# Optimization experiments

Hardware: AMD Instinct MI355X
Metric: run time of the kernel (lower is better)

Reference implementation:

```python
import jax, jax.numpy as jnp
import numpy as np

NEG = jnp.float32(-1e30)  # max-plus identity (finite to keep grads clean)


def setup_inputs() -> dict:
    key = jax.random.key(0)
    k1, k2 = jax.random.split(key)
    B, Cin, H, W = 8, 64, 64, 64
    Cout, kH, kW = 64, 3, 3
    x = jax.random.normal(k1, (B, Cin, H, W), dtype=jnp.float32)
    weight = jax.random.normal(k2, (Cout, Cin, kH, kW), dtype=jnp.float32)
    return {"x": x, "weight": weight, "kernel_size": 3, "padding": 1}


def reference(x, weight, kernel_size, padding):
    # Max-plus correlation (tropical conv), stride 1:
    #   out[b,co,y,x] = max_{ci,i,j} ( x_pad[b,ci,y+i,x+j] + weight[co,ci,i,j] )
    kH = kW = int(kernel_size)
    padH = padW = int(padding)
    B, Cin, H, W = x.shape
    Cout = weight.shape[0]
    xp = jnp.pad(x, ((0, 0), (0, 0), (padH, padH), (padW, padW)),
                 constant_values=NEG)  # -inf-like padding: identity of max
    Ho = H + 2 * padH - kH + 1
    Wo = W + 2 * padW - kW + 1
    out = jnp.full((B, Cout, Ho, Wo), NEG, dtype=x.dtype)
    for i in range(kH):          # small fixed kernel loop (kH*kW taps)
        for j in range(kW):
            win = xp[:, :, i:i + Ho, j:j + Wo]            # [B,Ci,Ho,Wo]
            cand = win[:, None] + weight[None, :, :, i, j, None, None]
            out = jnp.maximum(out, cand.max(axis=2))      # reduce over Ci
    return out
```

## Files before the change

kernel.cpp:

```cpp
#include <hip/hip_runtime.h>

#define NEGV -1e30f

constexpr int Bn = 8, Ci = 64, Hn = 64, Wn = 64, Co = 64;

constexpr int COB = 8;
constexpr int HT  = 4;

__global__ __launch_bounds__(256, 4)
void maxconv_kernel(const float* __restrict__ x, const float* __restrict__ wt,
                    float* __restrict__ out) {
    const int lane = threadIdx.x & 63;
    const int wrow = threadIdx.x >> 6;
    const int co0  = blockIdx.x * COB;
    const int h    = blockIdx.y * HT + wrow;
    const int b    = blockIdx.z;

    const int cl = lane > 0      ? lane - 1 : 0;
    const int cr = lane < Wn - 1 ? lane + 1 : Wn - 1;
    const bool edgeL = (lane == 0);
    const bool edgeR = (lane == Wn - 1);
    const bool hasUp = (h > 0);
    const bool hasDn = (h < Hn - 1);

    float acc[COB];
#pragma unroll
    for (int c = 0; c < COB; c++) acc[c] = NEGV;

    const float* p = x + ((size_t)b * Ci * Hn + h) * Wn;

    for (int ci = 0; ci < Ci; ci++, p += Hn * Wn) {
        float lm1 = NEGV, xm1 = NEGV, rm1 = NEGV;
        float lp1 = NEGV, xp1 = NEGV, rp1 = NEGV;
        if (hasUp) { lm1 = p[cl - Wn]; xm1 = p[lane - Wn]; rm1 = p[cr - Wn]; }
        if (hasDn) { lp1 = p[cl + Wn]; xp1 = p[lane + Wn]; rp1 = p[cr + Wn]; }
        float l0 = p[cl], x0 = p[lane], r0 = p[cr];

        if (edgeL) { lm1 = NEGV; l0 = NEGV; lp1 = NEGV; }
        if (edgeR) { rm1 = NEGV; r0 = NEGV; rp1 = NEGV; }

#pragma unroll
        for (int c = 0; c < COB; c++) {
            const float* wp = wt + ((size_t)(co0 + c) * Ci + ci) * 9;
            float t0 = lm1 + wp[0];
            float t1 = xm1 + wp[1];
            float t2 = rm1 + wp[2];
            float t3 = l0  + wp[3];
            float t4 = x0  + wp[4];
            float t5 = r0  + wp[5];
            float t6 = lp1 + wp[6];
            float t7 = xp1 + wp[7];
            float t8 = rp1 + wp[8];
            float a = acc[c];
            a = fmaxf(a, fmaxf(t0, t1));
            a = fmaxf(a, fmaxf(t2, t3));
            a = fmaxf(a, fmaxf(t4, t5));
            a = fmaxf(a, fmaxf(t6, t7));
            a = fmaxf(a, t8);
            acc[c] = a;
        }
    }

#pragma unroll
    for (int c = 0; c < COB; c++) {
        out[(((size_t)b * Co + co0 + c) * Hn + h) * Wn + lane] = acc[c];
    }
}

extern "C" void kernel_launch(void* const* d_in, const int* in_sizes, int n_in,
                              void* d_out, int out_size, void* d_ws, size_t ws_size,
                              hipStream_t stream) {
    const float* x  = (const float*)d_in[0];
    const float* wt = (const float*)d_in[1];
    float* out = (float*)d_out;

    dim3 grid(Co / COB, Hn / HT, Bn);
    maxconv_kernel<<<grid, 256, 0, stream>>>(x, wt, out);
}
```

Baseline: 125.4 us.

## Remap lanes to output channels with wave-uniform input loads and transposed weights

Restructures the work split so each wavefront lane handles one output channel while the wave covers a 4-wide strip of output columns. The input window values are then wave-uniform and can be scalar-loaded. A separate pre-pass transposes the weights so that per-lane weight loads are coalesced across output channels. Results are written as float4 stores. The aim is to drop the redundant per-channel weight loads and the divergent edge handling of the old layout, at the cost of an extra small kernel launch, workspace use, and output stores strided across channels.

```diff
diff --git a/kernel.cpp b/kernel.cpp
--- a/kernel.cpp
+++ b/kernel.cpp
@@ -4,67 +4,102 @@
 
 constexpr int Bn = 8, Ci = 64, Hn = 64, Wn = 64, Co = 64;
 
-constexpr int COB = 8;
-constexpr int HT  = 4;
+constexpr int G  = 4;
+constexpr int CW = Wn / G;
 
-__global__ __launch_bounds__(256, 4)
-void maxconv_kernel(const float* __restrict__ x, const float* __restrict__ wt,
-                    float* __restrict__ out) {
-    const int lane = threadIdx.x & 63;
-    const int wrow = threadIdx.x >> 6;
-    const int co0  = blockIdx.x * COB;
-    const int h    = blockIdx.y * HT + wrow;
-    const int b    = blockIdx.z;
+__global__ __launch_bounds__(256)
+void wtrans_kernel(const float* __restrict__ wt, float* __restrict__ wT) {
+    int idx = blockIdx.x * 256 + threadIdx.x;
+    if (idx < Ci * 9 * Co) {
+        int co = idx & 63;
+        int k  = (idx >> 6) % 9;
+        int ci = idx / (9 * Co);
+        wT[idx] = wt[((size_t)co * Ci + ci) * 9 + k];
+    }
+}
 
-    const int cl = lane > 0      ? lane - 1 : 0;
-    const int cr = lane < Wn - 1 ? lane + 1 : Wn - 1;
-    const bool edgeL = (lane == 0);
-    const bool edgeR = (lane == Wn - 1);
+template<int EDGE>
+__device__ __forceinline__ void load6(float* xv, const float* __restrict__ p) {
+    if (EDGE == 1) {
+        xv[0] = NEGV;
+#pragma unroll
+        for (int c = 1; c < 6; c++) xv[c] = p[c - 1];
+    } else if (EDGE == 2) {
+#pragma unroll
+        for (int c = 0; c < 5; c++) xv[c] = p[c];
+        xv[5] = NEGV;
+    } else {
+#pragma unroll
+        for (int c = 0; c < 6; c++) xv[c] = p[c];
+    }
+}
+
+template<int EDGE>
+__device__ __forceinline__ void run_wave(const float* __restrict__ x,
+                                         const float* __restrict__ wT,
+                                         float* __restrict__ out,
+                                         int b, int h, int w0, int lane) {
     const bool hasUp = (h > 0);
     const bool hasDn = (h < Hn - 1);
+    const int  cb    = (EDGE == 1) ? 0 : (w0 - 1);
 
-    float acc[COB];
+    const float* px = x + (((size_t)b * Ci) * Hn + h) * Wn + cb;
+    const float* pw = wT + lane;
+
+    float a[G];
 #pragma unroll
-    for (int c = 0; c < COB; c++) acc[c] = NEGV;
+    for (int p = 0; p < G; p++) a[p] = NEGV;
 
-    const float* p = x + ((size_t)b * Ci * Hn + h) * Wn;
+    for (int ci = 0; ci < Ci; ci++, px += Hn * Wn, pw += 9 * Co) {
+        float xu[6], xc[6], xd[6];
+        load6<EDGE>(xc, px);
+        if (hasUp) load6<EDGE>(xu, px - Wn);
+        else {
+#pragma unroll
+            for (int c = 0; c < 6; c++) xu[c] = NEGV;
+        }
+        if (hasDn) load6<EDGE>(xd, px + Wn);
+        else {
+#pragma unroll
+            for (int c = 0; c < 6; c++) xd[c] = NEGV;
+        }
 
-    for (int ci = 0; ci < Ci; ci++, p += Hn * Wn) {
-        float lm1 = NEGV, xm1 = NEGV, rm1 = NEGV;
-        float lp1 = NEGV, xp1 = NEGV, rp1 = NEGV;
-        if (hasUp) { lm1 = p[cl - Wn]; xm1 = p[lane - Wn]; rm1 = p[cr - Wn]; }
-        if (hasDn) { lp1 = p[cl + Wn]; xp1 = p[lane + Wn]; rp1 = p[cr + Wn]; }
-        float l0 = p[cl], x0 = p[lane], r0 = p[cr];
-
-        if (edgeL) { lm1 = NEGV; l0 = NEGV; lp1 = NEGV; }
-        if (edgeR) { rm1 = NEGV; r0 = NEGV; rp1 = NEGV; }
+        float wv[9];
+#pragma unroll
+        for (int k = 0; k < 9; k++) wv[k] = pw[k * Co];
 
 #pragma unroll
-        for (int c = 0; c < COB; c++) {
-            const float* wp = wt + ((size_t)(co0 + c) * Ci + ci) * 9;
-            float t0 = lm1 + wp[0];
-            float t1 = xm1 + wp[1];
-            float t2 = rm1 + wp[2];
-            float t3 = l0  + wp[3];
-            float t4 = x0  + wp[4];
-            float t5 = r0  + wp[5];
-            float t6 = lp1 + wp[6];
-            float t7 = xp1 + wp[7];
-            float t8 = rp1 + wp[8];
-            float a = acc[c];
-            a = fmaxf(a, fmaxf(t0, t1));
-            a = fmaxf(a, fmaxf(t2, t3));
-            a = fmaxf(a, fmaxf(t4, t5));
-            a = fmaxf(a, fmaxf(t6, t7));
-            a = fmaxf(a, t8);
-            acc[c] = a;
+        for (int p = 0; p < G; p++) {
+            float t0 = xu[p] + wv[0], t1 = xu[p + 1] + wv[1], t2 = xu[p + 2] + wv[2];
+            float t3 = xc[p] + wv[3], t4 = xc[p + 1] + wv[4], t5 = xc[p + 2] + wv[5];
+            float t6 = xd[p] + wv[6], t7 = xd[p + 1] + wv[7], t8 = xd[p + 2] + wv[8];
+            float v = a[p];
+            v = fmaxf(v, fmaxf(t0, t1));
+            v = fmaxf(v, fmaxf(t2, t3));
+            v = fmaxf(v, fmaxf(t4, t5));
+            v = fmaxf(v, fmaxf(t6, t7));
+            v = fmaxf(v, t8);
+            a[p] = v;
         }
     }
 
-#pragma unroll
-    for (int c = 0; c < COB; c++) {
-        out[(((size_t)b * Co + co0 + c) * Hn + h) * Wn + lane] = acc[c];
-    }
+    float4 st = make_float4(a[0], a[1], a[2], a[3]);
+    *reinterpret_cast<float4*>(out + (((size_t)b * Co + lane) * Hn + h) * Wn + w0) = st;
+}
+
+__global__ __launch_bounds__(256, 8)
+void maxconv_main(const float* __restrict__ x, const float* __restrict__ wT,
+                  float* __restrict__ out) {
+    const int lane = threadIdx.x & 63;
+    const int wid  = threadIdx.x >> 6;
+    const int cw   = __builtin_amdgcn_readfirstlane(blockIdx.x * 4 + wid);
+    const int w0   = cw * G;
+    const int h    = blockIdx.y;
+    const int b    = blockIdx.z;
+
+    if (cw == 0)           run_wave<1>(x, wT, out, b, h, w0, lane);
+    else if (cw == CW - 1) run_wave<2>(x, wT, out, b, h, w0, lane);
+    else                   run_wave<0>(x, wT, out, b, h, w0, lane);
 }
 
 extern "C" void kernel_launch(void* const* d_in, const int* in_sizes, int n_in,
@@ -73,7 +108,10 @@
     const float* x  = (const float*)d_in[0];
     const float* wt = (const float*)d_in[1];
     float* out = (float*)d_out;
+    float* wT  = (float*)d_ws;
 
-    dim3 grid(Co / COB, Hn / HT, Bn);
-    maxconv_kernel<<<grid, 256, 0, stream>>>(x, wt, out);
+    wtrans_kernel<<<(Ci * 9 * Co + 255) / 256, 256, 0, stream>>>(wt, wT);
+
+    dim3 grid(CW / 4, Hn, Bn);
+    maxconv_main<<<grid, 256, 0, stream>>>(x, wT, out);
 }
```

Result: faster. 122.8 us (-2.1%).

## Stage weights in LDS, double-buffer input loads, use v_max3 reductions

Applied to the files above, without the earlier changes.

Each block now copies its 8 output channels' weights into shared memory, padded to 12 floats per 3x3 tap set so they can be read as float4 vectors, in place of scalar global weight loads per ci. The Ci loop is unrolled by two with ping-pong register buffers, so the next channel's input loads are issued before the current channel's arithmetic. Max reductions use inline v_max3_f32 to cut instruction count, and the 3D grid is flattened to 1D with output-channel groups as the outermost index. The cost is 24 KB of LDS per block, which can limit occupancy, plus a staging loop and barrier at block start.

```diff
diff --git a/kernel.cpp b/kernel.cpp
--- a/kernel.cpp
+++ b/kernel.cpp
@@ -7,64 +7,109 @@
 constexpr int COB = 8;
 constexpr int HT  = 4;
 
+__device__ __forceinline__ float vmax3(float a, float b, float c) {
+    float d;
+    asm("v_max3_f32 %0, %1, %2, %3" : "=v"(d) : "v"(a), "v"(b), "v"(c));
+    return d;
+}
+
+struct X9 { float um, uc, ur, cm, cc, cr, dm, dc, dr; };
+
+__device__ __forceinline__ void loadX(X9& v, const float* __restrict__ p,
+                                      int cl, int lane, int cr,
+                                      bool hasUp, bool hasDn) {
+    v.cm = p[cl]; v.cc = p[lane]; v.cr = p[cr];
+    if (hasUp) { v.um = p[cl - Wn]; v.uc = p[lane - Wn]; v.ur = p[cr - Wn]; }
+    else       { v.um = NEGV;      v.uc = NEGV;          v.ur = NEGV; }
+    if (hasDn) { v.dm = p[cl + Wn]; v.dc = p[lane + Wn]; v.dr = p[cr + Wn]; }
+    else       { v.dm = NEGV;      v.dc = NEGV;          v.dr = NEGV; }
+}
+
+__device__ __forceinline__ void edgefix(X9& v, bool eL, bool eR) {
+    v.um = eL ? NEGV : v.um; v.cm = eL ? NEGV : v.cm; v.dm = eL ? NEGV : v.dm;
+    v.ur = eR ? NEGV : v.ur; v.cr = eR ? NEGV : v.cr; v.dr = eR ? NEGV : v.dr;
+}
+
+__device__ __forceinline__ void computeC(float* acc, const X9& v,
+                                         const float* __restrict__ lwp) {
+#pragma unroll
+    for (int c = 0; c < COB; c++) {
+        const float4 wa = *reinterpret_cast<const float4*>(lwp + c * 12);
+        const float4 wb = *reinterpret_cast<const float4*>(lwp + c * 12 + 4);
+        const float  w8 = lwp[c * 12 + 8];
+        float t0 = v.um + wa.x, t1 = v.uc + wa.y, t2 = v.ur + wa.z;
+        float t3 = v.cm + wa.w, t4 = v.cc + wb.x, t5 = v.cr + wb.y;
+        float t6 = v.dm + wb.z, t7 = v.dc + wb.w, t8 = v.dr + w8;
+        float m0 = vmax3(t0, t1, t2);
+        float m1 = vmax3(t3, t4, t5);
+        float m2 = vmax3(t6, t7, t8);
+        acc[c] = vmax3(acc[c], m0, m1);
+        acc[c] = fmaxf(acc[c], m2);
+    }
+}
+
 __global__ __launch_bounds__(256, 4)
-void maxconv_kernel(const float* __restrict__ x, const float* __restrict__ wt,
-                    float* __restrict__ out) {
-    const int lane = threadIdx.x & 63;
-    const int wrow = threadIdx.x >> 6;
-    const int co0  = blockIdx.x * COB;
-    const int h    = blockIdx.y * HT + wrow;
-    const int b    = blockIdx.z;
+void maxconv_main(const float* __restrict__ x, const float* __restrict__ wt,
+                  float* __restrict__ out) {
+    __shared__ __align__(16) float lw[Ci * COB * 12];
 
-    const int cl = lane > 0      ? lane - 1 : 0;
-    const int cr = lane < Wn - 1 ? lane + 1 : Wn - 1;
-    const bool edgeL = (lane == 0);
-    const bool edgeR = (lane == Wn - 1);
+    const int tid  = threadIdx.x;
+    const int lane = tid & 63;
+    const int wrow = tid >> 6;
+
+    const int id = blockIdx.x;
+    const int g  = id >> 7;
+    const int c  = id & 127;
+    const int b  = c >> 4;
+    const int hq = c & 15;
+    const int h  = hq * HT + wrow;
+    const int co0 = g * COB;
+
+    const float* wg = wt + (size_t)co0 * Ci * 9;
+    for (int t = tid; t < Ci * COB * 9; t += 256) {
+        int cl  = t / (Ci * 9);
+        int rem = t - cl * (Ci * 9);
+        int ci  = rem / 9;
+        int k   = rem - ci * 9;
+        lw[(ci * COB + cl) * 12 + k] = wg[t];
+    }
+    __syncthreads();
+
+    const int  cl = lane > 0      ? lane - 1 : 0;
+    const int  cr = lane < Wn - 1 ? lane + 1 : Wn - 1;
+    const bool eL = (lane == 0);
+    const bool eR = (lane == Wn - 1);
     const bool hasUp = (h > 0);
     const bool hasDn = (h < Hn - 1);
 
+    const float* p = x + ((size_t)b * Ci * Hn + h) * Wn;
+
     float acc[COB];
 #pragma unroll
-    for (int c = 0; c < COB; c++) acc[c] = NEGV;
+    for (int q = 0; q < COB; q++) acc[q] = NEGV;
 
-    const float* p = x + ((size_t)b * Ci * Hn + h) * Wn;
+    X9 xA, xB;
 
-    for (int ci = 0; ci < Ci; ci++, p += Hn * Wn) {
-        float lm1 = NEGV, xm1 = NEGV, rm1 = NEGV;
-        float lp1 = NEGV, xp1 = NEGV, rp1 = NEGV;
-        if (hasUp) { lm1 = p[cl - Wn]; xm1 = p[lane - Wn]; rm1 = p[cr - Wn]; }
-        if (hasDn) { lp1 = p[cl + Wn]; xp1 = p[lane + Wn]; rp1 = p[cr + Wn]; }
-        float l0 = p[cl], x0 = p[lane], r0 = p[cr];
+    loadX(xA, p, cl, lane, cr, hasUp, hasDn);  p += Hn * Wn;
 
-        if (edgeL) { lm1 = NEGV; l0 = NEGV; lp1 = NEGV; }
-        if (edgeR) { rm1 = NEGV; r0 = NEGV; rp1 = NEGV; }
+#pragma unroll 1
+    for (int ci = 0; ci < Ci - 2; ci += 2) {
+        loadX(xB, p, cl, lane, cr, hasUp, hasDn);  p += Hn * Wn;
+        edgefix(xA, eL, eR);
+        computeC(acc, xA, lw + ci * (COB * 12));
+        loadX(xA, p, cl, lane, cr, hasUp, hasDn);  p += Hn * Wn;
+        edgefix(xB, eL, eR);
+        computeC(acc, xB, lw + (ci + 1) * (COB * 12));
+    }
+    loadX(xB, p, cl, lane, cr, hasUp, hasDn);
+    edgefix(xA, eL, eR);
+    computeC(acc, xA, lw + 62 * (COB * 12));
+    edgefix(xB, eL, eR);
+    computeC(acc, xB, lw + 63 * (COB * 12));
 
+    float* po = out + (((size_t)b * Co + co0) * Hn + h) * Wn + lane;
 #pragma unroll
-        for (int c = 0; c < COB; c++) {
-            const float* wp = wt + ((size_t)(co0 + c) * Ci + ci) * 9;
-            float t0 = lm1 + wp[0];
-            float t1 = xm1 + wp[1];
-            float t2 = rm1 + wp[2];
-            float t3 = l0  + wp[3];
-            float t4 = x0  + wp[4];
-            float t5 = r0  + wp[5];
-            float t6 = lp1 + wp[6];
-            float t7 = xp1 + wp[7];
-            float t8 = rp1 + wp[8];
-            float a = acc[c];
-            a = fmaxf(a, fmaxf(t0, t1));
-            a = fmaxf(a, fmaxf(t2, t3));
-            a = fmaxf(a, fmaxf(t4, t5));
-            a = fmaxf(a, fmaxf(t6, t7));
-            a = fmaxf(a, t8);
-            acc[c] = a;
-        }
-    }
-
-#pragma unroll
-    for (int c = 0; c < COB; c++) {
-        out[(((size_t)b * Co + co0 + c) * Hn + h) * Wn + lane] = acc[c];
-    }
+    for (int q = 0; q < COB; q++) po[(size_t)q * Hn * Wn] = acc[q];
 }
 
 extern "C" void kernel_launch(void* const* d_in, const int* in_sizes, int n_in,
@@ -74,6 +119,5 @@
     const float* wt = (const float*)d_in[1];
     float* out = (float*)d_out;
 
-    dim3 grid(Co / COB, Hn / HT, Bn);
-    maxconv_kernel<<<grid, 256, 0, stream>>>(x, wt, out);
+    maxconv_main<<<1024, 256, 0, stream>>>(x, wt, out);
 }
```

Result: no change. 126.5 us (+0.8%).
